# Optimization experiments

Hardware: AMD Instinct MI355X
Metric: run time of the kernel (lower is better)

The kernel has to match this reference:

```python
import jax, jax.numpy as jnp
import numpy as np

NUM_HEADS = 32
NUM_KV_HEADS = 8
HEAD_SIZE = 128
SCALE = 0.08838834764831845  # 1/sqrt(128)
BATCH = 32
MAX_BLOCKS_PER_SEQ = 128
BLOCK_SIZE = 16
NUM_BLOCKS = BATCH * MAX_BLOCKS_PER_SEQ  # 4096
MAX_CTX = MAX_BLOCKS_PER_SEQ * BLOCK_SIZE  # 2048


def setup_inputs() -> dict:
    key = jax.random.key(0)
    ks = jax.random.split(key, 8)
    query = jax.random.normal(ks[0], (BATCH, 1, NUM_HEADS * HEAD_SIZE), dtype=jnp.float32)
    k_new = jax.random.normal(ks[1], (BATCH, 1, NUM_KV_HEADS * HEAD_SIZE), dtype=jnp.float32)
    v_new = jax.random.normal(ks[2], (BATCH, 1, NUM_KV_HEADS * HEAD_SIZE), dtype=jnp.float32)
    key_cache = jax.random.normal(ks[3], (NUM_BLOCKS, NUM_KV_HEADS, HEAD_SIZE, BLOCK_SIZE), dtype=jnp.float32)
    value_cache = jax.random.normal(ks[4], (NUM_BLOCKS, NUM_KV_HEADS, HEAD_SIZE, BLOCK_SIZE), dtype=jnp.float32)
    # each sequence owns a contiguous stripe of blocks, accessed through the table
    block_tables = jnp.arange(NUM_BLOCKS, dtype=jnp.int32).reshape(BATCH, MAX_BLOCKS_PER_SEQ)
    context_lens = jax.random.randint(ks[5], (BATCH,), 1, MAX_CTX + 1, dtype=jnp.int32)
    # slot for the newly-decoded token (position context_len-1)
    last = context_lens - 1
    blk_idx = block_tables[jnp.arange(BATCH), last // BLOCK_SIZE]
    slot_mapping = (blk_idx * BLOCK_SIZE + last % BLOCK_SIZE).reshape(BATCH, 1).astype(jnp.int32)
    return {
        "query": query, "key": k_new, "value": v_new,
        "key_cache": key_cache, "value_cache": value_cache,
        "block_tables": block_tables, "context_lens": context_lens,
        "slot_mapping": slot_mapping,
    }


def reference(query, key, value, key_cache, value_cache, block_tables, context_lens, slot_mapping):
    B = query.shape[0]
    block_size = value_cache.shape[3]
    q_per_kv = NUM_HEADS // NUM_KV_HEADS

    # --- reshape_and_cache: write new k/v into paged caches at slot_mapping ---
    slots = slot_mapping.reshape(-1)                       # [B] (seq_len=1 decode)
    blk = slots // block_size
    off = slots % block_size
    k_new = key.reshape(B, NUM_KV_HEADS, HEAD_SIZE)
    v_new = value.reshape(B, NUM_KV_HEADS, HEAD_SIZE)
    key_cache = key_cache.at[blk, :, :, off].set(k_new)
    value_cache = value_cache.at[blk, :, :, off].set(v_new)

    # --- paged_attention_v1: gather blocks via block_tables, masked softmax ---
    # [B, MB, KVH, D, bs] -> [B, MB, bs, KVH, D] -> [B, T, KVH, D]
    K = jnp.moveaxis(key_cache[block_tables], -1, 2).reshape(B, -1, NUM_KV_HEADS, HEAD_SIZE)
    V = jnp.moveaxis(value_cache[block_tables], -1, 2).reshape(B, -1, NUM_KV_HEADS, HEAD_SIZE)
    T = K.shape[1]

    q = query.reshape(B, NUM_KV_HEADS, q_per_kv, HEAD_SIZE)
    scores = jnp.einsum('bkqd,btkd->bkqt', q, K) * SCALE   # [B, KVH, Qper, T]
    valid = (jnp.arange(T, dtype=jnp.int32)[None, :] < context_lens[:, None])
    scores = jnp.where(valid[:, None, None, :], scores, jnp.finfo(scores.dtype).min)
    probs = jax.nn.softmax(scores, axis=-1)
    out = jnp.einsum('bkqt,btkd->bkqd', probs, V)          # [B, KVH, Qper, D]
    return out.reshape(B, 1, NUM_HEADS * HEAD_SIZE)
```

## Files before the change

kernel.cpp:

```cpp
#include <hip/hip_runtime.h>
#include <float.h>

#define NUM_HEADS    32
#define NUM_KV_HEADS 8
#define HEAD_SIZE    128
#define Q_PER_KV     4
#define BLOCK_SZ     16
#define MAX_BLOCKS   128
#define MAX_CTX      2048
#define SCALE        0.08838834764831845f

typedef float v4f __attribute__((ext_vector_type(4)));

__global__ __launch_bounds__(512, 2)
void paged_attn_kernel(const float* __restrict__ query,
                       const float* __restrict__ k_new,
                       const float* __restrict__ v_new,
                       const float* __restrict__ key_cache,
                       const float* __restrict__ value_cache,
                       const int* __restrict__ block_tables,
                       const int* __restrict__ context_lens,
                       float* __restrict__ out) {
    const int h   = blockIdx.x;
    const int b   = blockIdx.y;
    const int tid = threadIdx.x;

    __shared__ float q_lds[Q_PER_KV * HEAD_SIZE];
    __shared__ float s_lds[Q_PER_KV * MAX_CTX];
    __shared__ float red_lds[4 * Q_PER_KV * HEAD_SIZE];
    __shared__ float inv_lds[Q_PER_KV];

    const int ctx  = context_lens[b];
    const int nb   = (ctx + BLOCK_SZ - 1) / BLOCK_SZ;
    const int last = ctx - 1;

    {
        const int qh = tid >> 7, d = tid & 127;
        q_lds[tid] = query[((size_t)b * NUM_HEADS + h * Q_PER_KV + qh) * HEAD_SIZE + d] * SCALE;
    }
    __syncthreads();

    {
        const int bi = tid >> 2;
        const int o  = tid & 3;
        if (bi < nb) {
            const int phys = block_tables[b * MAX_BLOCKS + bi];
            const v4f* kp = reinterpret_cast<const v4f*>(key_cache) +
                            ((size_t)phys * NUM_KV_HEADS + h) * (HEAD_SIZE * BLOCK_SZ / 4);
            const v4f* q4 = reinterpret_cast<const v4f*>(q_lds);
            v4f acc[Q_PER_KV];
            #pragma unroll
            for (int qh = 0; qh < Q_PER_KV; ++qh) acc[qh] = (v4f)0.f;

            #pragma unroll 4
            for (int d4 = 0; d4 < HEAD_SIZE / 4; ++d4) {
                v4f k[4];
                #pragma unroll
                for (int dd = 0; dd < 4; ++dd) k[dd] = kp[d4 * 16 + dd * 4 + o];
                #pragma unroll
                for (int qh = 0; qh < Q_PER_KV; ++qh) {
                    v4f qv = q4[qh * (HEAD_SIZE / 4) + d4];
                    #pragma unroll
                    for (int dd = 0; dd < 4; ++dd) acc[qh] += qv[dd] * k[dd];
                }
            }
            const int t0 = bi * BLOCK_SZ + o * 4;
            #pragma unroll
            for (int qh = 0; qh < Q_PER_KV; ++qh) {
                v4f sv;
                #pragma unroll
                for (int j = 0; j < 4; ++j)
                    sv[j] = (t0 + j < ctx) ? acc[qh][j] : -FLT_MAX;
                *reinterpret_cast<v4f*>(&s_lds[qh * MAX_CTX + t0]) = sv;
            }
        }
    }
    __syncthreads();

    if (tid < 4 * 64) {
        const int w = tid >> 6, lane = tid & 63;
        const float* kn = k_new + ((size_t)b * NUM_KV_HEADS + h) * HEAD_SIZE;
        float v = q_lds[w * HEAD_SIZE + lane] * kn[lane] +
                  q_lds[w * HEAD_SIZE + lane + 64] * kn[lane + 64];
        #pragma unroll
        for (int off = 32; off; off >>= 1) v += __shfl_xor(v, off);
        if (lane == 0) s_lds[w * MAX_CTX + last] = v;
    }
    __syncthreads();

    if (tid < 4 * 64) {
        const int w = tid >> 6, lane = tid & 63;
        const int T = nb * BLOCK_SZ;
        float m = -FLT_MAX;
        for (int t = lane; t < T; t += 64) m = fmaxf(m, s_lds[w * MAX_CTX + t]);
        #pragma unroll
        for (int off = 32; off; off >>= 1) m = fmaxf(m, __shfl_xor(m, off));
        float sum = 0.f;
        for (int t = lane; t < T; t += 64) {
            float e = __expf(s_lds[w * MAX_CTX + t] - m);
            s_lds[w * MAX_CTX + t] = e;
            sum += e;
        }
        #pragma unroll
        for (int off = 32; off; off >>= 1) sum += __shfl_xor(sum, off);
        if (lane == 0) inv_lds[w] = 1.0f / sum;
    }
    __syncthreads();

    float pl[Q_PER_KV];
    #pragma unroll
    for (int qh = 0; qh < Q_PER_KV; ++qh) pl[qh] = s_lds[qh * MAX_CTX + last];
    __syncthreads();
    if (tid < Q_PER_KV) s_lds[tid * MAX_CTX + last] = 0.f;
    __syncthreads();

    {
        const int d   = tid & 127;
        const int seg = tid >> 7;
        float acc[Q_PER_KV] = {0.f, 0.f, 0.f, 0.f};

        for (int bi = seg; bi < nb; bi += 4) {
            const int phys = block_tables[b * MAX_BLOCKS + bi];
            const v4f* vp = reinterpret_cast<const v4f*>(value_cache) +
                            ((size_t)phys * NUM_KV_HEADS + h) * (HEAD_SIZE * BLOCK_SZ / 4);
            v4f vv[4];
            #pragma unroll
            for (int j = 0; j < 4; ++j) vv[j] = vp[d * 4 + j];
            #pragma unroll
            for (int qh = 0; qh < Q_PER_KV; ++qh) {
                const v4f* pq = reinterpret_cast<const v4f*>(&s_lds[qh * MAX_CTX + bi * BLOCK_SZ]);
                #pragma unroll
                for (int j = 0; j < 4; ++j) {
                    v4f p = pq[j];
                    acc[qh] += p[0] * vv[j][0] + p[1] * vv[j][1] +
                               p[2] * vv[j][2] + p[3] * vv[j][3];
                }
            }
        }

        if (seg == 0) {
            const float vn = v_new[((size_t)b * NUM_KV_HEADS + h) * HEAD_SIZE + d];
            #pragma unroll
            for (int qh = 0; qh < Q_PER_KV; ++qh) acc[qh] += pl[qh] * vn;
        }

        #pragma unroll
        for (int qh = 0; qh < Q_PER_KV; ++qh)
            red_lds[(seg * Q_PER_KV + qh) * HEAD_SIZE + d] = acc[qh];
    }
    __syncthreads();

    {
        const int qh = tid >> 7, d = tid & 127;
        float r = red_lds[(0 * Q_PER_KV + qh) * HEAD_SIZE + d] +
                  red_lds[(1 * Q_PER_KV + qh) * HEAD_SIZE + d] +
                  red_lds[(2 * Q_PER_KV + qh) * HEAD_SIZE + d] +
                  red_lds[(3 * Q_PER_KV + qh) * HEAD_SIZE + d];
        out[((size_t)b * NUM_HEADS + h * Q_PER_KV + qh) * HEAD_SIZE + d] = r * inv_lds[qh];
    }
}

extern "C" void kernel_launch(void* const* d_in, const int* in_sizes, int n_in,
                              void* d_out, int out_size, void* d_ws, size_t ws_size,
                              hipStream_t stream) {
    const float* query       = (const float*)d_in[0];
    const float* k_new       = (const float*)d_in[1];
    const float* v_new       = (const float*)d_in[2];
    const float* key_cache   = (const float*)d_in[3];
    const float* value_cache = (const float*)d_in[4];
    const int*   block_tables  = (const int*)d_in[5];
    const int*   context_lens  = (const int*)d_in[6];
    float* out = (float*)d_out;

    const int batch = in_sizes[6];
    dim3 grid(NUM_KV_HEADS, batch);
    paged_attn_kernel<<<grid, 512, 0, stream>>>(query, k_new, v_new,
                                                key_cache, value_cache,
                                                block_tables, context_lens, out);
}
```

Measured before the change: 72.27 us.

## Split paged attention into context chunks with a separate log-sum-exp reduce kernel

Replaces the single per-(batch, kv-head) workgroup with a flash-decoding split: each 64-thread workgroup handles a 256-token chunk, computes partial max, sum and unnormalised output into workspace, and a second kernel merges the chunks and folds in the new token. This raises the number of workgroups from 256 to up to 2048, so more CUs are busy and context-length imbalance across sequences matters less. The cost is a second launch, workspace traffic, and small 64-thread workgroups that each reload q.

```diff
diff --git a/kernel.cpp b/kernel.cpp
--- a/kernel.cpp
+++ b/kernel.cpp
@@ -10,39 +10,49 @@
 #define MAX_CTX      2048
 #define SCALE        0.08838834764831845f
 
+#define CHUNK_BLOCKS 16
+#define CHUNK_TOK    (CHUNK_BLOCKS * BLOCK_SZ)
+#define NCHUNK       (MAX_BLOCKS / CHUNK_BLOCKS)
+#define WS_STRIDE    (2 * Q_PER_KV + Q_PER_KV * HEAD_SIZE)
+
 typedef float v4f __attribute__((ext_vector_type(4)));
 
-__global__ __launch_bounds__(512, 2)
-void paged_attn_kernel(const float* __restrict__ query,
-                       const float* __restrict__ k_new,
-                       const float* __restrict__ v_new,
-                       const float* __restrict__ key_cache,
-                       const float* __restrict__ value_cache,
-                       const int* __restrict__ block_tables,
-                       const int* __restrict__ context_lens,
-                       float* __restrict__ out) {
+__global__ __launch_bounds__(64, 8)
+void paged_attn_chunk(const float* __restrict__ query,
+                      const float* __restrict__ key_cache,
+                      const float* __restrict__ value_cache,
+                      const int* __restrict__ block_tables,
+                      const int* __restrict__ context_lens,
+                      float* __restrict__ ws) {
     const int h   = blockIdx.x;
     const int b   = blockIdx.y;
+    const int c   = blockIdx.z;
     const int tid = threadIdx.x;
-
-    __shared__ float q_lds[Q_PER_KV * HEAD_SIZE];
-    __shared__ float s_lds[Q_PER_KV * MAX_CTX];
-    __shared__ float red_lds[4 * Q_PER_KV * HEAD_SIZE];
-    __shared__ float inv_lds[Q_PER_KV];
 
     const int ctx  = context_lens[b];
     const int nb   = (ctx + BLOCK_SZ - 1) / BLOCK_SZ;
+    const int cb   = c * CHUNK_BLOCKS;
+    if (cb >= nb) return;
     const int last = ctx - 1;
 
-    {
-        const int qh = tid >> 7, d = tid & 127;
-        q_lds[tid] = query[((size_t)b * NUM_HEADS + h * Q_PER_KV + qh) * HEAD_SIZE + d] * SCALE;
-    }
-    __syncthreads();
-
-    {
-        const int bi = tid >> 2;
-        const int o  = tid & 3;
+    __shared__ float q_lds[Q_PER_KV * HEAD_SIZE];
+    __shared__ float s_lds[Q_PER_KV * CHUNK_TOK];
+    __shared__ float ml_lds[2 * Q_PER_KV];
+
+    {
+        const v4f* qg = reinterpret_cast<const v4f*>(
+            query + ((size_t)b * NUM_HEADS + h * Q_PER_KV) * HEAD_SIZE);
+        v4f* ql = reinterpret_cast<v4f*>(q_lds);
+        ql[tid]      = qg[tid]      * SCALE;
+        ql[tid + 64] = qg[tid + 64] * SCALE;
+    }
+    __syncthreads();
+
+    {
+        const int bil = tid >> 2;
+        const int o   = tid & 3;
+        const int bi  = cb + bil;
+        const int t0  = bil * BLOCK_SZ + o * 4;
         if (bi < nb) {
             const int phys = block_tables[b * MAX_BLOCKS + bi];
             const v4f* kp = reinterpret_cast<const v4f*>(key_cache) +
@@ -51,7 +61,6 @@
             v4f acc[Q_PER_KV];
             #pragma unroll
             for (int qh = 0; qh < Q_PER_KV; ++qh) acc[qh] = (v4f)0.f;
-
             #pragma unroll 4
             for (int d4 = 0; d4 < HEAD_SIZE / 4; ++d4) {
                 v4f k[4];
@@ -64,100 +73,137 @@
                     for (int dd = 0; dd < 4; ++dd) acc[qh] += qv[dd] * k[dd];
                 }
             }
-            const int t0 = bi * BLOCK_SZ + o * 4;
+            const int g0 = c * CHUNK_TOK + t0;
             #pragma unroll
             for (int qh = 0; qh < Q_PER_KV; ++qh) {
                 v4f sv;
                 #pragma unroll
-                for (int j = 0; j < 4; ++j)
-                    sv[j] = (t0 + j < ctx) ? acc[qh][j] : -FLT_MAX;
-                *reinterpret_cast<v4f*>(&s_lds[qh * MAX_CTX + t0]) = sv;
+                for (int j = 0; j < 4; ++j) {
+                    const int g = g0 + j;
+                    sv[j] = (g < ctx && g != last) ? acc[qh][j] : -FLT_MAX;
+                }
+                *reinterpret_cast<v4f*>(&s_lds[qh * CHUNK_TOK + t0]) = sv;
             }
+        } else {
+            const v4f mv = (v4f)(-FLT_MAX);
+            #pragma unroll
+            for (int qh = 0; qh < Q_PER_KV; ++qh)
+                *reinterpret_cast<v4f*>(&s_lds[qh * CHUNK_TOK + t0]) = mv;
         }
     }
     __syncthreads();
 
-    if (tid < 4 * 64) {
-        const int w = tid >> 6, lane = tid & 63;
-        const float* kn = k_new + ((size_t)b * NUM_KV_HEADS + h) * HEAD_SIZE;
-        float v = q_lds[w * HEAD_SIZE + lane] * kn[lane] +
-                  q_lds[w * HEAD_SIZE + lane + 64] * kn[lane + 64];
-        #pragma unroll
-        for (int off = 32; off; off >>= 1) v += __shfl_xor(v, off);
-        if (lane == 0) s_lds[w * MAX_CTX + last] = v;
-    }
-    __syncthreads();
-
-    if (tid < 4 * 64) {
-        const int w = tid >> 6, lane = tid & 63;
-        const int T = nb * BLOCK_SZ;
-        float m = -FLT_MAX;
-        for (int t = lane; t < T; t += 64) m = fmaxf(m, s_lds[w * MAX_CTX + t]);
+    float* wsp = ws + (((size_t)b * NUM_KV_HEADS + h) * NCHUNK + c) * WS_STRIDE;
+    #pragma unroll
+    for (int qh = 0; qh < Q_PER_KV; ++qh) {
+        float s0 = s_lds[qh * CHUNK_TOK + tid];
+        float s1 = s_lds[qh * CHUNK_TOK + tid + 64];
+        float s2 = s_lds[qh * CHUNK_TOK + tid + 128];
+        float s3 = s_lds[qh * CHUNK_TOK + tid + 192];
+        float m = fmaxf(fmaxf(s0, s1), fmaxf(s2, s3));
         #pragma unroll
         for (int off = 32; off; off >>= 1) m = fmaxf(m, __shfl_xor(m, off));
-        float sum = 0.f;
-        for (int t = lane; t < T; t += 64) {
-            float e = __expf(s_lds[w * MAX_CTX + t] - m);
-            s_lds[w * MAX_CTX + t] = e;
-            sum += e;
-        }
-        #pragma unroll
-        for (int off = 32; off; off >>= 1) sum += __shfl_xor(sum, off);
-        if (lane == 0) inv_lds[w] = 1.0f / sum;
-    }
-    __syncthreads();
-
-    float pl[Q_PER_KV];
-    #pragma unroll
-    for (int qh = 0; qh < Q_PER_KV; ++qh) pl[qh] = s_lds[qh * MAX_CTX + last];
-    __syncthreads();
-    if (tid < Q_PER_KV) s_lds[tid * MAX_CTX + last] = 0.f;
-    __syncthreads();
-
-    {
-        const int d   = tid & 127;
-        const int seg = tid >> 7;
-        float acc[Q_PER_KV] = {0.f, 0.f, 0.f, 0.f};
-
-        for (int bi = seg; bi < nb; bi += 4) {
-            const int phys = block_tables[b * MAX_BLOCKS + bi];
+        float p0 = (s0 == -FLT_MAX) ? 0.f : __expf(s0 - m);
+        float p1 = (s1 == -FLT_MAX) ? 0.f : __expf(s1 - m);
+        float p2 = (s2 == -FLT_MAX) ? 0.f : __expf(s2 - m);
+        float p3 = (s3 == -FLT_MAX) ? 0.f : __expf(s3 - m);
+        s_lds[qh * CHUNK_TOK + tid]       = p0;
+        s_lds[qh * CHUNK_TOK + tid + 64]  = p1;
+        s_lds[qh * CHUNK_TOK + tid + 128] = p2;
+        s_lds[qh * CHUNK_TOK + tid + 192] = p3;
+        float l = p0 + p1 + p2 + p3;
+        #pragma unroll
+        for (int off = 32; off; off >>= 1) l += __shfl_xor(l, off);
+        if (tid == 0) { ml_lds[qh] = m; ml_lds[Q_PER_KV + qh] = l; }
+    }
+    __syncthreads();
+    if (tid < 2 * Q_PER_KV) wsp[tid] = ml_lds[tid];
+
+    {
+        const int d0 = tid, d1 = tid + 64;
+        float acc0[Q_PER_KV] = {0.f, 0.f, 0.f, 0.f};
+        float acc1[Q_PER_KV] = {0.f, 0.f, 0.f, 0.f};
+        const int nbl = min(nb - cb, CHUNK_BLOCKS);
+        for (int bil = 0; bil < nbl; ++bil) {
+            const int phys = block_tables[b * MAX_BLOCKS + cb + bil];
             const v4f* vp = reinterpret_cast<const v4f*>(value_cache) +
                             ((size_t)phys * NUM_KV_HEADS + h) * (HEAD_SIZE * BLOCK_SZ / 4);
-            v4f vv[4];
-            #pragma unroll
-            for (int j = 0; j < 4; ++j) vv[j] = vp[d * 4 + j];
+            v4f vv0[4], vv1[4];
+            #pragma unroll
+            for (int j = 0; j < 4; ++j) { vv0[j] = vp[d0 * 4 + j]; vv1[j] = vp[d1 * 4 + j]; }
             #pragma unroll
             for (int qh = 0; qh < Q_PER_KV; ++qh) {
-                const v4f* pq = reinterpret_cast<const v4f*>(&s_lds[qh * MAX_CTX + bi * BLOCK_SZ]);
+                const v4f* pq = reinterpret_cast<const v4f*>(
+                    &s_lds[qh * CHUNK_TOK + bil * BLOCK_SZ]);
                 #pragma unroll
                 for (int j = 0; j < 4; ++j) {
                     v4f p = pq[j];
-                    acc[qh] += p[0] * vv[j][0] + p[1] * vv[j][1] +
-                               p[2] * vv[j][2] + p[3] * vv[j][3];
+                    acc0[qh] += p[0]*vv0[j][0] + p[1]*vv0[j][1] + p[2]*vv0[j][2] + p[3]*vv0[j][3];
+                    acc1[qh] += p[0]*vv1[j][0] + p[1]*vv1[j][1] + p[2]*vv1[j][2] + p[3]*vv1[j][3];
                 }
             }
         }
-
-        if (seg == 0) {
-            const float vn = v_new[((size_t)b * NUM_KV_HEADS + h) * HEAD_SIZE + d];
-            #pragma unroll
-            for (int qh = 0; qh < Q_PER_KV; ++qh) acc[qh] += pl[qh] * vn;
+        float* wo = wsp + 2 * Q_PER_KV;
+        #pragma unroll
+        for (int qh = 0; qh < Q_PER_KV; ++qh) {
+            wo[qh * HEAD_SIZE + d0] = acc0[qh];
+            wo[qh * HEAD_SIZE + d1] = acc1[qh];
         }
-
-        #pragma unroll
-        for (int qh = 0; qh < Q_PER_KV; ++qh)
-            red_lds[(seg * Q_PER_KV + qh) * HEAD_SIZE + d] = acc[qh];
-    }
-    __syncthreads();
-
-    {
-        const int qh = tid >> 7, d = tid & 127;
-        float r = red_lds[(0 * Q_PER_KV + qh) * HEAD_SIZE + d] +
-                  red_lds[(1 * Q_PER_KV + qh) * HEAD_SIZE + d] +
-                  red_lds[(2 * Q_PER_KV + qh) * HEAD_SIZE + d] +
-                  red_lds[(3 * Q_PER_KV + qh) * HEAD_SIZE + d];
-        out[((size_t)b * NUM_HEADS + h * Q_PER_KV + qh) * HEAD_SIZE + d] = r * inv_lds[qh];
-    }
+    }
+}
+
+__global__ __launch_bounds__(512, 2)
+void paged_attn_reduce(const float* __restrict__ query,
+                       const float* __restrict__ k_new,
+                       const float* __restrict__ v_new,
+                       const int* __restrict__ context_lens,
+                       const float* __restrict__ ws,
+                       float* __restrict__ out) {
+    const int h   = blockIdx.x;
+    const int b   = blockIdx.y;
+    const int tid = threadIdx.x;
+
+    __shared__ float snew_lds[Q_PER_KV];
+
+    const int ctx = context_lens[b];
+    const int nb  = (ctx + BLOCK_SZ - 1) / BLOCK_SZ;
+    const int nch = (nb + CHUNK_BLOCKS - 1) / CHUNK_BLOCKS;
+
+    if (tid < 4 * 64) {
+        const int w = tid >> 6, lane = tid & 63;
+        const float* qp = query + ((size_t)b * NUM_HEADS + h * Q_PER_KV + w) * HEAD_SIZE;
+        const float* kn = k_new + ((size_t)b * NUM_KV_HEADS + h) * HEAD_SIZE;
+        float v = qp[lane] * kn[lane] + qp[lane + 64] * kn[lane + 64];
+        #pragma unroll
+        for (int off = 32; off; off >>= 1) v += __shfl_xor(v, off);
+        if (lane == 0) snew_lds[w] = v * SCALE;
+    }
+    __syncthreads();
+
+    const int qh = tid >> 7, d = tid & 127;
+    const float* wsb = ws + ((size_t)b * NUM_KV_HEADS + h) * NCHUNK * WS_STRIDE;
+
+    float M = -FLT_MAX, L = 0.f, acc = 0.f;
+    for (int c = 0; c < nch; ++c) {
+        const float* wsp = wsb + (size_t)c * WS_STRIDE;
+        const float mc = wsp[qh];
+        const float lc = wsp[Q_PER_KV + qh];
+        const float oc = wsp[2 * Q_PER_KV + qh * HEAD_SIZE + d];
+        const float nM = fmaxf(M, mc);
+        const float eM = __expf(M - nM), ec = __expf(mc - nM);
+        acc = acc * eM + oc * ec;
+        L   = L   * eM + lc * ec;
+        M   = nM;
+    }
+    {
+        const float s  = snew_lds[qh];
+        const float nM = fmaxf(M, s);
+        const float eM = __expf(M - nM), es = __expf(s - nM);
+        const float vn = v_new[((size_t)b * NUM_KV_HEADS + h) * HEAD_SIZE + d];
+        acc = acc * eM + es * vn;
+        L   = L   * eM + es;
+    }
+    out[((size_t)b * NUM_HEADS + h * Q_PER_KV + qh) * HEAD_SIZE + d] = acc / L;
 }
 
 extern "C" void kernel_launch(void* const* d_in, const int* in_sizes, int n_in,
@@ -171,10 +217,14 @@
     const int*   block_tables  = (const int*)d_in[5];
     const int*   context_lens  = (const int*)d_in[6];
     float* out = (float*)d_out;
+    float* ws  = (float*)d_ws;
 
     const int batch = in_sizes[6];
-    dim3 grid(NUM_KV_HEADS, batch);
-    paged_attn_kernel<<<grid, 512, 0, stream>>>(query, k_new, v_new,
-                                                key_cache, value_cache,
-                                                block_tables, context_lens, out);
+
+    dim3 g1(NUM_KV_HEADS, batch, NCHUNK);
+    paged_attn_chunk<<<g1, 64, 0, stream>>>(query, key_cache, value_cache,
+                                            block_tables, context_lens, ws);
+    dim3 g2(NUM_KV_HEADS, batch);
+    paged_attn_reduce<<<g2, 512, 0, stream>>>(query, k_new, v_new,
+                                              context_lens, ws, out);
 }
```

Result: faster. 65.68 us (-9.1%).
